# Performance work log

Hardware: AMD Instinct MI355X
Metric: run time of the kernel (lower is better)

The kernel has to match this reference:

```python
import jax, jax.numpy as jnp
import numpy as np

NUM_HEADS = 12
ALPHA = 0.5
TANH_CLIP = 5.0


def setup_inputs() -> dict:
    key = jax.random.key(0)
    k1, k2, k3, k4, k5 = jax.random.split(key, 5)
    B, N, C = 8, 1024, 768
    x = jax.random.normal(k1, (B, N, C), dtype=jnp.float32)
    # qkv: Linear(C -> 3C), proj: Linear(C -> C); torch stores weight as [out, in]
    s = 1.0 / np.sqrt(C)
    qkv_w = jax.random.normal(k2, (3 * C, C), dtype=jnp.float32) * s
    qkv_b = jax.random.normal(k3, (3 * C,), dtype=jnp.float32) * 0.02
    proj_w = jax.random.normal(k4, (C, C), dtype=jnp.float32) * s
    proj_b = jax.random.normal(k5, (C,), dtype=jnp.float32) * 0.02
    return {"x": x, "qkv_w": qkv_w, "qkv_b": qkv_b, "proj_w": proj_w, "proj_b": proj_b}


def reference(x, qkv_w, qkv_b, proj_w, proj_b):
    B, N, C = x.shape
    H = NUM_HEADS
    D = C // H
    scale = D ** -0.5
    # qkv projection -> [B, N, 3, H, D] -> q/k/v each [B, H, N, D]
    qkv = (x @ qkv_w.T + qkv_b).reshape(B, N, 3, H, D)
    qkv = jnp.transpose(qkv, (2, 0, 3, 1, 4))
    q, k, v = qkv[0], qkv[1], qkv[2]
    # pre-softmax scores [B, H, N, N]
    scores = jnp.einsum("bhnd,bhmd->bhnm", q * scale, k)
    scores_t = jnp.swapaxes(scores, -2, -1)
    scores_sym = 0.5 * (scores + scores_t)
    scores_asym = 0.5 * (scores - scores_t)
    scores = scores_sym + ALPHA * scores_asym
    # gamma_mode == 'approx'
    gamma = np.sqrt((1.0 + ALPHA ** 2) / 2.0)
    scores = scores / gamma
    # tanh clip
    scores = TANH_CLIP * jnp.tanh(scores / TANH_CLIP)
    attn = jax.nn.softmax(scores, axis=-1)
    out = jnp.einsum("bhnm,bhmd->bhnd", attn, v)  # [B, H, N, D]
    out = jnp.transpose(out, (0, 2, 1, 3)).reshape(B, N, C)
    return out @ proj_w.T + proj_b
```

## Files before the change

### kernel.cpp

```cpp
#include <hip/hip_runtime.h>
#include <hip/hip_bf16.h>
#include <stdint.h>

typedef unsigned short u16;
typedef __attribute__((ext_vector_type(8))) short bf16x8;
typedef __attribute__((ext_vector_type(4))) float f32x4;

#define LDS_AS(p) ((__attribute__((address_space(3))) void*)(p))
#define GLB_AS(p) ((__attribute__((address_space(1))) void*)(p))

__device__ __forceinline__ u16 f2bf(float f) {
  union { float f; uint32_t u; } v; v.f = f;
  uint32_t u = v.u;
  u += 0x7fffu + ((u >> 16) & 1u);
  return (u16)(u >> 16);
}

__device__ __forceinline__ float exp2_fast(float x) {
  float r;
  asm("v_exp_f32 %0, %1" : "=v"(r) : "v"(x));
  return r;
}

__device__ __forceinline__ float bits2f(uint32_t u) {
  union { uint32_t u; float f; } v; v.u = u; return v.f;
}
__device__ __forceinline__ uint32_t f2bits(float f) {
  union { float f; uint32_t u; } v; v.f = f; return v.u;
}

__device__ __forceinline__ void cvt8(const float* __restrict__ s, u16* __restrict__ d) {
  const float4* sv = (const float4*)s;
  float4 a = sv[0], b = sv[1];
  uint4 o;
  o.x = (uint32_t)f2bf(a.x) | ((uint32_t)f2bf(a.y) << 16);
  o.y = (uint32_t)f2bf(a.z) | ((uint32_t)f2bf(a.w) << 16);
  o.z = (uint32_t)f2bf(b.x) | ((uint32_t)f2bf(b.y) << 16);
  o.w = (uint32_t)f2bf(b.z) | ((uint32_t)f2bf(b.w) << 16);
  *(uint4*)d = o;
}

__global__ __launch_bounds__(256) void k_convert(
    const float* __restrict__ x, const float* __restrict__ wq, const float* __restrict__ wp,
    u16* __restrict__ xb, u16* __restrict__ wqb, u16* __restrict__ wpb) {
  int tid = blockIdx.x * 256 + threadIdx.x;
  int np  = gridDim.x * 256;
  for (int i = tid; i < (8192*768)/8; i += np) cvt8(x  + (size_t)i*8, xb  + (size_t)i*8);
  for (int i = tid; i < (2304*768)/8; i += np) cvt8(wq + (size_t)i*8, wqb + (size_t)i*8);
  for (int i = tid; i < (768*768)/8;  i += np) cvt8(wp + (size_t)i*8, wpb + (size_t)i*8);
}

template<bool SWAP>
__device__ __forceinline__ void gemm_core(const u16* __restrict__ A,
                                          const u16* __restrict__ B,
                                          u16* As, u16* Bs,
                                          int rowA0, int rowB0,
                                          f32x4 acc[4][4]) {
  const int t  = threadIdx.x;
  const int lane = t & 63;
  const int wv = t >> 6;
  const int wr = wv >> 1, wc = wv & 1;
  const int lr = lane & 15, lg = lane >> 4;

#pragma unroll 1
  for (int kt = 0; kt < 24; ++kt) {
    const int k0 = kt * 32;
    __syncthreads();
#pragma unroll
    for (int p = 0; p < 2; ++p) {
      int idx = p * 256 + t;
      int row = idx >> 2;
      int cc  = (idx & 3) ^ ((row >> 1) & 3);
      __builtin_amdgcn_global_load_lds(GLB_AS(A + (size_t)(rowA0 + row) * 768 + k0 + cc * 8),
                                       LDS_AS(As + idx * 8), 16, 0, 0);
    }
#pragma unroll
    for (int p = 0; p < 2; ++p) {
      int idx = p * 256 + t;
      int row = idx >> 2;
      int cc  = (idx & 3) ^ ((row >> 1) & 3);
      __builtin_amdgcn_global_load_lds(GLB_AS(B + (size_t)(rowB0 + row) * 768 + k0 + cc * 8),
                                       LDS_AS(Bs + idx * 8), 16, 0, 0);
    }
    asm volatile("s_waitcnt vmcnt(0)" ::: "memory");
    __syncthreads();

    bf16x8 af[4], bf_[4];
#pragma unroll
    for (int mi = 0; mi < 4; ++mi) {
      int row = wr * 64 + mi * 16 + lr;
      int cc  = lg ^ ((row >> 1) & 3);
      af[mi] = *(const bf16x8*)(As + row * 32 + cc * 8);
    }
#pragma unroll
    for (int ni = 0; ni < 4; ++ni) {
      int row = wc * 64 + ni * 16 + lr;
      int cc  = lg ^ ((row >> 1) & 3);
      bf_[ni] = *(const bf16x8*)(Bs + row * 32 + cc * 8);
    }
#pragma unroll
    for (int mi = 0; mi < 4; ++mi)
#pragma unroll
      for (int ni = 0; ni < 4; ++ni) {
        if (SWAP)
          acc[mi][ni] = __builtin_amdgcn_mfma_f32_16x16x32_bf16(bf_[ni], af[mi], acc[mi][ni], 0, 0, 0);
        else
          acc[mi][ni] = __builtin_amdgcn_mfma_f32_16x16x32_bf16(af[mi], bf_[ni], acc[mi][ni], 0, 0, 0);
      }
  }
}

__global__ __launch_bounds__(256) void k_gemm_qkv(
    const u16* __restrict__ Aq, const u16* __restrict__ Bw, const float* __restrict__ bias,
    u16* __restrict__ Qh, u16* __restrict__ Kh, u16* __restrict__ Vt) {
  __shared__ u16 As[128 * 32];
  __shared__ u16 Bs[128 * 32];
  int bid = blockIdx.x;
  int wg  = (bid & 7) * 144 + (bid >> 3);
  int bx  = wg % 18, by = wg / 18;

  const int t = threadIdx.x, lane = t & 63, wv = t >> 6;
  const int wr = wv >> 1, wc = wv & 1, lr = lane & 15, lg = lane >> 4;
  const int tsec = bx / 6;
  const int colBase = bx * 128 + wc * 64;

  const float gam = 0.7905694150420949f;
  const float sc1 = __builtin_sqrtf(0.09375f / gam);
  const float sc2 = __builtin_sqrtf(0.03125f / gam);

  f32x4 acc[4][4];
#pragma unroll
  for (int mi = 0; mi < 4; ++mi)
#pragma unroll
    for (int ni = 0; ni < 4; ++ni) acc[mi][ni] = (f32x4){0.f, 0.f, 0.f, 0.f};

  if (tsec < 2) {
    gemm_core<true>(Aq, Bw, As, Bs, by * 128, bx * 128, acc);

    float4 bv4[4];
#pragma unroll
    for (int ni = 0; ni < 4; ++ni)
      bv4[ni] = *(const float4*)(bias + colBase + ni * 16 + lg * 4);

#pragma unroll
    for (int mi = 0; mi < 4; ++mi) {
      int n = by * 128 + wr * 64 + mi * 16 + lr;
      int b = n >> 10, nn = n & 1023;
#pragma unroll
      for (int ni = 0; ni < 4; ++ni) {
        int fs = colBase - tsec * 768 + ni * 16 + lg * 4;
        int h = fs >> 6, d = fs & 63;
        size_t rowq = ((size_t)(b * 12 + h) * 1024 + nn) * 128;
        float v0 = acc[mi][ni][0] + bv4[ni].x;
        float v1 = acc[mi][ni][1] + bv4[ni].y;
        float v2 = acc[mi][ni][2] + bv4[ni].z;
        float v3 = acc[mi][ni][3] + bv4[ni].w;
        uint2 wq_, wk_;
        wq_.x = (uint32_t)f2bf(v0 * sc1) | ((uint32_t)f2bf(v1 * sc1) << 16);
        wq_.y = (uint32_t)f2bf(v2 * sc1) | ((uint32_t)f2bf(v3 * sc1) << 16);
        wk_.x = (uint32_t)f2bf(v0 * sc2) | ((uint32_t)f2bf(v1 * sc2) << 16);
        wk_.y = (uint32_t)f2bf(v2 * sc2) | ((uint32_t)f2bf(v3 * sc2) << 16);
        if (tsec == 0) {
          *(uint2*)(Qh + rowq + d)      = wq_;
          *(uint2*)(Kh + rowq + 64 + d) = wk_;
        } else {
          *(uint2*)(Kh + rowq + d)      = wq_;
          *(uint2*)(Qh + rowq + 64 + d) = wk_;
        }
      }
    }
  } else {
    gemm_core<false>(Aq, Bw, As, Bs, by * 128, bx * 128, acc);

    float bv[4];
#pragma unroll
    for (int ni = 0; ni < 4; ++ni) bv[ni] = bias[colBase + ni * 16 + lr];

#pragma unroll
    for (int mi = 0; mi < 4; ++mi) {
      int tok0 = by * 128 + wr * 64 + mi * 16 + lg * 4;
      int b = tok0 >> 10, n0 = tok0 & 1023;
#pragma unroll
      for (int ni = 0; ni < 4; ++ni) {
        int fs = colBase - 2 * 768 + ni * 16 + lr;
        int h = fs >> 6, d = fs & 63;
        float v0 = acc[mi][ni][0] + bv[ni];
        float v1 = acc[mi][ni][1] + bv[ni];
        float v2 = acc[mi][ni][2] + bv[ni];
        float v3 = acc[mi][ni][3] + bv[ni];
        uint2 w;
        w.x = (uint32_t)f2bf(v0) | ((uint32_t)f2bf(v1) << 16);
        w.y = (uint32_t)f2bf(v2) | ((uint32_t)f2bf(v3) << 16);
        *(uint2*)(Vt + ((size_t)((b * 12 + h) * 64 + d)) * 1024 + n0) = w;
      }
    }
  }
}

__global__ __launch_bounds__(256, 4) void k_attn(
    const u16* __restrict__ Qh, const u16* __restrict__ Kh, const u16* __restrict__ Vt,
    u16* __restrict__ attn) {
  __shared__ u16 Ks[2][32 * 128];
  __shared__ u16 Vs[2][64 * 32];
  __shared__ u16 Ps[4][32 * 40];

  int bid = blockIdx.x;
  int wg = (bid & 7) * 96 + (bid >> 3);
  int bh = wg >> 3, qb = wg & 7;
  int b = bh / 12, h = bh % 12;

  const int t = threadIdx.x, lane = t & 63, wv = t >> 6;
  const int lr = lane & 15, lg = lane >> 4;

  const size_t khb = (size_t)bh * 1024 * 128;
  const size_t vtb = (size_t)bh * 64 * 1024;

  bf16x8 qf[2][4];
  {
    const u16* qp = Qh + ((size_t)bh * 1024 + qb * 128 + wv * 32 + lr) * 128 + lg * 8;
#pragma unroll
    for (int it = 0; it < 2; ++it)
#pragma unroll
      for (int kk = 0; kk < 4; ++kk)
        qf[it][kk] = *(const bf16x8*)(qp + it * 16 * 128 + kk * 32);
  }

#define STAGE(KT, BUF)                                                                         \
  {                                                                                            \
    _Pragma("unroll")                                                                          \
    for (int p = 0; p < 2; ++p) {                                                              \
      int idx = p * 256 + t;                                                                   \
      int row = idx >> 4;                                                                      \
      int cc  = (idx & 15) ^ (row & 7);                                                        \
      __builtin_amdgcn_global_load_lds(GLB_AS(Kh + khb + (size_t)((KT) * 32 + row) * 128 + cc * 8), \
                                       LDS_AS(Ks[BUF] + idx * 8), 16, 0, 0);                   \
    }                                                                                          \
    {                                                                                          \
      int d = t >> 2;                                                                          \
      int g = (t & 3) ^ ((d + (d >> 2)) & 3);                                                  \
      __builtin_amdgcn_global_load_lds(GLB_AS(Vt + vtb + (size_t)d * 1024 + (KT) * 32 + g * 8),\
                                       LDS_AS(Vs[BUF] + t * 8), 16, 0, 0);                     \
    }                                                                                          \
  }

  STAGE(0, 0);

  f32x4 acc_o[4][2];
#pragma unroll
  for (int dt = 0; dt < 4; ++dt)
#pragma unroll
    for (int it = 0; it < 2; ++it) acc_o[dt][it] = (f32x4){0.f, 0.f, 0.f, 0.f};
  float dsum[2] = {0.f, 0.f};

  u16* pw = Ps[wv];
  const float C1 = 0.57707801636f;
  const float C2 = -14.4269504089f;

#pragma unroll 1
  for (int kt = 0; kt < 32; ++kt) {
    const int cur = kt & 1;
    __syncthreads();

    if (kt < 31) STAGE(kt + 1, cur ^ 1);

    const u16* K0 = Ks[cur];
    f32x4 accs[2][2];
#pragma unroll
    for (int jt = 0; jt < 2; ++jt)
#pragma unroll
      for (int it = 0; it < 2; ++it) accs[jt][it] = (f32x4){0.f, 0.f, 0.f, 0.f};
#pragma unroll
    for (int jt = 0; jt < 2; ++jt) {
#pragma unroll
      for (int kk = 0; kk < 4; ++kk) {
        int row = jt * 16 + lr;
        int cc  = (kk * 4 + lg) ^ (row & 7);
        bf16x8 kf = *(const bf16x8*)(K0 + row * 128 + cc * 8);
#pragma unroll
        for (int it = 0; it < 2; ++it)
          accs[jt][it] = __builtin_amdgcn_mfma_f32_16x16x32_bf16(kf, qf[it][kk], accs[jt][it], 0, 0, 0);
      }
    }

#pragma unroll
    for (int jt = 0; jt < 2; ++jt) {
#pragma unroll
      for (int it = 0; it < 2; ++it) {
        float p0 = exp2_fast(C2 * __builtin_amdgcn_rcpf(exp2_fast(C1 * accs[jt][it][0]) + 1.0f));
        float p1 = exp2_fast(C2 * __builtin_amdgcn_rcpf(exp2_fast(C1 * accs[jt][it][1]) + 1.0f));
        float p2 = exp2_fast(C2 * __builtin_amdgcn_rcpf(exp2_fast(C1 * accs[jt][it][2]) + 1.0f));
        float p3 = exp2_fast(C2 * __builtin_amdgcn_rcpf(exp2_fast(C1 * accs[jt][it][3]) + 1.0f));
        uint32_t a0 = f2bits(p0), a1 = f2bits(p1), a2 = f2bits(p2), a3 = f2bits(p3);
        uint2 w;
        w.x = (a0 >> 16) | (a1 & 0xFFFF0000u);
        w.y = (a2 >> 16) | (a3 & 0xFFFF0000u);
        dsum[it] += (bits2f(a0 & 0xFFFF0000u) + bits2f(a1 & 0xFFFF0000u))
                  + (bits2f(a2 & 0xFFFF0000u) + bits2f(a3 & 0xFFFF0000u));
        *(uint2*)(pw + (it * 16 + lr) * 40 + jt * 16 + lg * 4) = w;
      }
    }

    asm volatile("" ::: "memory");

    {
      const u16* V0 = Vs[cur];
      bf16x8 pa[2];
#pragma unroll
      for (int it = 0; it < 2; ++it)
        pa[it] = *(const bf16x8*)(pw + (it * 16 + lr) * 40 + lg * 8);
#pragma unroll
      for (int dt = 0; dt < 4; ++dt) {
        int row = dt * 16 + lr;
        int ph  = lg ^ ((row + (row >> 2)) & 3);
        bf16x8 vf = *(const bf16x8*)(V0 + row * 32 + ph * 8);
#pragma unroll
        for (int it = 0; it < 2; ++it)
          acc_o[dt][it] = __builtin_amdgcn_mfma_f32_16x16x32_bf16(vf, pa[it], acc_o[dt][it], 0, 0, 0);
      }
    }
  }
#undef STAGE

  float rinv[2];
#pragma unroll
  for (int it = 0; it < 2; ++it) {
    float v = dsum[it];
    v += __shfl_xor(v, 16);
    v += __shfl_xor(v, 32);
    rinv[it] = __builtin_amdgcn_rcpf(v);
  }

#pragma unroll
  for (int dt = 0; dt < 4; ++dt) {
#pragma unroll
    for (int it = 0; it < 2; ++it) {
      float v0 = acc_o[dt][it][0] * rinv[it];
      float v1 = acc_o[dt][it][1] * rinv[it];
      float v2 = acc_o[dt][it][2] * rinv[it];
      float v3 = acc_o[dt][it][3] * rinv[it];
      uint2 w;
      w.x = (uint32_t)f2bf(v0) | ((uint32_t)f2bf(v1) << 16);
      w.y = (uint32_t)f2bf(v2) | ((uint32_t)f2bf(v3) << 16);
      int n = qb * 128 + wv * 32 + it * 16 + lr;
      *(uint2*)(attn + ((size_t)(b * 1024 + n)) * 768 + h * 64 + dt * 16 + lg * 4) = w;
    }
  }
}

__global__ __launch_bounds__(256) void k_gemm_proj(
    const u16* __restrict__ Ain, const u16* __restrict__ Bw, const float* __restrict__ bias,
    float* __restrict__ out) {
  __shared__ u16 As[128 * 32];
  __shared__ u16 Bs[128 * 32];
  int bid = blockIdx.x;
  int wg  = (bid & 7) * 48 + (bid >> 3);
  int bx  = wg % 6, by = wg / 6;

  f32x4 acc[4][4];
#pragma unroll
  for (int mi = 0; mi < 4; ++mi)
#pragma unroll
    for (int ni = 0; ni < 4; ++ni) acc[mi][ni] = (f32x4){0.f, 0.f, 0.f, 0.f};

  gemm_core<false>(Ain, Bw, As, Bs, by * 128, bx * 128, acc);

  const int t = threadIdx.x, lane = t & 63, wv = t >> 6;
  const int wr = wv >> 1, wc = wv & 1, lr = lane & 15, lg = lane >> 4;
  const int col0 = bx * 128 + wc * 64;

  float bv[4];
#pragma unroll
  for (int ni = 0; ni < 4; ++ni) bv[ni] = bias[col0 + ni * 16 + lr];

#pragma unroll
  for (int mi = 0; mi < 4; ++mi) {
    int tok0 = by * 128 + wr * 64 + mi * 16 + lg * 4;
#pragma unroll
    for (int ni = 0; ni < 4; ++ni) {
      int col = col0 + ni * 16 + lr;
#pragma unroll
      for (int r = 0; r < 4; ++r) {
        out[(size_t)(tok0 + r) * 768 + col] = acc[mi][ni][r] + bv[ni];
      }
    }
  }
}

extern "C" void kernel_launch(void* const* d_in, const int* in_sizes, int n_in,
                              void* d_out, int out_size, void* d_ws, size_t ws_size,
                              hipStream_t stream) {
  (void)in_sizes; (void)n_in; (void)out_size;
  const float* x      = (const float*)d_in[0];
  const float* qkv_w  = (const float*)d_in[1];
  const float* qkv_b  = (const float*)d_in[2];
  const float* proj_w = (const float*)d_in[3];
  const float* proj_b = (const float*)d_in[4];
  float* out = (float*)d_out;

  uint8_t* ws = (uint8_t*)d_ws;
  u16* xb  = (u16*)(ws + 0);
  u16* wqb = (u16*)(ws + 12582912);
  u16* wpb = (u16*)(ws + 16121856);
  u16* Qh  = (u16*)(ws + 17301504);
  u16* Kh  = (u16*)(ws + 42467328);
  u16* Vt  = (u16*)(ws + 80216064);
  if (ws_size < 92798976) return;

  u16* attnb = xb;

  k_convert<<<1024, 256, 0, stream>>>(x, qkv_w, proj_w, xb, wqb, wpb);
  k_gemm_qkv<<<1152, 256, 0, stream>>>(xb, wqb, qkv_b, Qh, Kh, Vt);
  k_attn<<<768, 256, 0, stream>>>(Qh, Kh, Vt, attnb);
  k_gemm_proj<<<384, 256, 0, stream>>>(attnb, wpb, proj_b, out);
}
```

Before: 156.4 us.

## Halve attention query tile per block, double grid, fold tanh constant into QKV scale

The attention kernel now handles 64 queries per block (16 per wave) instead of 128, doubling the grid to 1536 blocks and raising the occupancy hint to 6 blocks per CU. The goal is better load balance across CUs and lower register pressure. The price is that each K/V tile is loaded from global memory twice as often. The tanh-clip constant C1 is now folded into the Q/K scaling in the QKV GEMM, which removes one multiply per score. The change also adds s_setprio around the MFMA sections and packs bf16 halves with a perm instruction.

```diff
diff --git a/kernel.cpp b/kernel.cpp
--- a/kernel.cpp
+++ b/kernel.cpp
@@ -27,6 +27,9 @@
 }
 __device__ __forceinline__ uint32_t f2bits(float f) {
   union { float f; uint32_t u; } v; v.f = f; return v.u;
+}
+__device__ __forceinline__ uint32_t pack_hi16(uint32_t lo_src, uint32_t hi_src) {
+  return __builtin_amdgcn_perm(hi_src, lo_src, 0x07060302u);
 }
 
 __device__ __forceinline__ void cvt8(const float* __restrict__ s, u16* __restrict__ d) {
@@ -125,8 +128,9 @@
   const int colBase = bx * 128 + wc * 64;
 
   const float gam = 0.7905694150420949f;
-  const float sc1 = __builtin_sqrtf(0.09375f / gam);
-  const float sc2 = __builtin_sqrtf(0.03125f / gam);
+  const float rC1 = __builtin_sqrtf(0.57707801636f);
+  const float sc1 = __builtin_sqrtf(0.09375f / gam) * rC1;
+  const float sc2 = __builtin_sqrtf(0.03125f / gam) * rC1;
 
   f32x4 acc[4][4];
 #pragma unroll
@@ -197,16 +201,16 @@
   }
 }
 
-__global__ __launch_bounds__(256, 4) void k_attn(
+__global__ __launch_bounds__(256, 6) void k_attn(
     const u16* __restrict__ Qh, const u16* __restrict__ Kh, const u16* __restrict__ Vt,
     u16* __restrict__ attn) {
   __shared__ u16 Ks[2][32 * 128];
   __shared__ u16 Vs[2][64 * 32];
-  __shared__ u16 Ps[4][32 * 40];
+  __shared__ u16 Ps[4][16 * 40];
 
   int bid = blockIdx.x;
-  int wg = (bid & 7) * 96 + (bid >> 3);
-  int bh = wg >> 3, qb = wg & 7;
+  int wg = (bid & 7) * 192 + (bid >> 3);
+  int bh = wg >> 4, qb = wg & 15;
   int b = bh / 12, h = bh % 12;
 
   const int t = threadIdx.x, lane = t & 63, wv = t >> 6;
@@ -215,14 +219,12 @@
   const size_t khb = (size_t)bh * 1024 * 128;
   const size_t vtb = (size_t)bh * 64 * 1024;
 
-  bf16x8 qf[2][4];
+  bf16x8 qf[4];
   {
-    const u16* qp = Qh + ((size_t)bh * 1024 + qb * 128 + wv * 32 + lr) * 128 + lg * 8;
-#pragma unroll
-    for (int it = 0; it < 2; ++it)
-#pragma unroll
-      for (int kk = 0; kk < 4; ++kk)
-        qf[it][kk] = *(const bf16x8*)(qp + it * 16 * 128 + kk * 32);
+    const u16* qp = Qh + ((size_t)bh * 1024 + qb * 64 + wv * 16 + lr) * 128 + lg * 8;
+#pragma unroll
+    for (int kk = 0; kk < 4; ++kk)
+      qf[kk] = *(const bf16x8*)(qp + kk * 32);
   }
 
 #define STAGE(KT, BUF)                                                                         \
@@ -245,15 +247,12 @@
 
   STAGE(0, 0);
 
-  f32x4 acc_o[4][2];
-#pragma unroll
-  for (int dt = 0; dt < 4; ++dt)
-#pragma unroll
-    for (int it = 0; it < 2; ++it) acc_o[dt][it] = (f32x4){0.f, 0.f, 0.f, 0.f};
-  float dsum[2] = {0.f, 0.f};
+  f32x4 acc_o[4];
+#pragma unroll
+  for (int dt = 0; dt < 4; ++dt) acc_o[dt] = (f32x4){0.f, 0.f, 0.f, 0.f};
+  float dsum = 0.f;
 
   u16* pw = Ps[wv];
-  const float C1 = 0.57707801636f;
   const float C2 = -14.4269504089f;
 
 #pragma unroll 1
@@ -264,11 +263,10 @@
     if (kt < 31) STAGE(kt + 1, cur ^ 1);
 
     const u16* K0 = Ks[cur];
-    f32x4 accs[2][2];
-#pragma unroll
-    for (int jt = 0; jt < 2; ++jt)
-#pragma unroll
-      for (int it = 0; it < 2; ++it) accs[jt][it] = (f32x4){0.f, 0.f, 0.f, 0.f};
+    f32x4 accs[2];
+#pragma unroll
+    for (int jt = 0; jt < 2; ++jt) accs[jt] = (f32x4){0.f, 0.f, 0.f, 0.f};
+    __builtin_amdgcn_s_setprio(1);
 #pragma unroll
     for (int jt = 0; jt < 2; ++jt) {
 #pragma unroll
@@ -276,74 +274,63 @@
         int row = jt * 16 + lr;
         int cc  = (kk * 4 + lg) ^ (row & 7);
         bf16x8 kf = *(const bf16x8*)(K0 + row * 128 + cc * 8);
-#pragma unroll
-        for (int it = 0; it < 2; ++it)
-          accs[jt][it] = __builtin_amdgcn_mfma_f32_16x16x32_bf16(kf, qf[it][kk], accs[jt][it], 0, 0, 0);
-      }
-    }
+        accs[jt] = __builtin_amdgcn_mfma_f32_16x16x32_bf16(kf, qf[kk], accs[jt], 0, 0, 0);
+      }
+    }
+    __builtin_amdgcn_s_setprio(0);
 
 #pragma unroll
     for (int jt = 0; jt < 2; ++jt) {
-#pragma unroll
-      for (int it = 0; it < 2; ++it) {
-        float p0 = exp2_fast(C2 * __builtin_amdgcn_rcpf(exp2_fast(C1 * accs[jt][it][0]) + 1.0f));
-        float p1 = exp2_fast(C2 * __builtin_amdgcn_rcpf(exp2_fast(C1 * accs[jt][it][1]) + 1.0f));
-        float p2 = exp2_fast(C2 * __builtin_amdgcn_rcpf(exp2_fast(C1 * accs[jt][it][2]) + 1.0f));
-        float p3 = exp2_fast(C2 * __builtin_amdgcn_rcpf(exp2_fast(C1 * accs[jt][it][3]) + 1.0f));
-        uint32_t a0 = f2bits(p0), a1 = f2bits(p1), a2 = f2bits(p2), a3 = f2bits(p3);
-        uint2 w;
-        w.x = (a0 >> 16) | (a1 & 0xFFFF0000u);
-        w.y = (a2 >> 16) | (a3 & 0xFFFF0000u);
-        dsum[it] += (bits2f(a0 & 0xFFFF0000u) + bits2f(a1 & 0xFFFF0000u))
-                  + (bits2f(a2 & 0xFFFF0000u) + bits2f(a3 & 0xFFFF0000u));
-        *(uint2*)(pw + (it * 16 + lr) * 40 + jt * 16 + lg * 4) = w;
-      }
+      float p0 = exp2_fast(C2 * __builtin_amdgcn_rcpf(exp2_fast(accs[jt][0]) + 1.0f));
+      float p1 = exp2_fast(C2 * __builtin_amdgcn_rcpf(exp2_fast(accs[jt][1]) + 1.0f));
+      float p2 = exp2_fast(C2 * __builtin_amdgcn_rcpf(exp2_fast(accs[jt][2]) + 1.0f));
+      float p3 = exp2_fast(C2 * __builtin_amdgcn_rcpf(exp2_fast(accs[jt][3]) + 1.0f));
+      uint32_t a0 = f2bits(p0), a1 = f2bits(p1), a2 = f2bits(p2), a3 = f2bits(p3);
+      uint2 w;
+      w.x = pack_hi16(a0, a1);
+      w.y = pack_hi16(a2, a3);
+      dsum += (bits2f(a0 & 0xFFFF0000u) + bits2f(a1 & 0xFFFF0000u))
+            + (bits2f(a2 & 0xFFFF0000u) + bits2f(a3 & 0xFFFF0000u));
+      *(uint2*)(pw + lr * 40 + jt * 16 + lg * 4) = w;
     }
 
     asm volatile("" ::: "memory");
 
     {
       const u16* V0 = Vs[cur];
-      bf16x8 pa[2];
-#pragma unroll
-      for (int it = 0; it < 2; ++it)
-        pa[it] = *(const bf16x8*)(pw + (it * 16 + lr) * 40 + lg * 8);
+      bf16x8 pa = *(const bf16x8*)(pw + lr * 40 + lg * 8);
+      __builtin_amdgcn_s_setprio(1);
 #pragma unroll
       for (int dt = 0; dt < 4; ++dt) {
         int row = dt * 16 + lr;
         int ph  = lg ^ ((row + (row >> 2)) & 3);
         bf16x8 vf = *(const bf16x8*)(V0 + row * 32 + ph * 8);
-#pragma unroll
-        for (int it = 0; it < 2; ++it)
-          acc_o[dt][it] = __builtin_amdgcn_mfma_f32_16x16x32_bf16(vf, pa[it], acc_o[dt][it], 0, 0, 0);
-      }
+        acc_o[dt] = __builtin_amdgcn_mfma_f32_16x16x32_bf16(vf, pa, acc_o[dt], 0, 0, 0);
+      }
+      __builtin_amdgcn_s_setprio(0);
     }
   }
 #undef STAGE
 
-  float rinv[2];
-#pragma unroll
-  for (int it = 0; it < 2; ++it) {
-    float v = dsum[it];
+  float rinv;
+  {
+    float v = dsum;
     v += __shfl_xor(v, 16);
     v += __shfl_xor(v, 32);
-    rinv[it] = __builtin_amdgcn_rcpf(v);
+    rinv = __builtin_amdgcn_rcpf(v);
   }
 
 #pragma unroll
   for (int dt = 0; dt < 4; ++dt) {
-#pragma unroll
-    for (int it = 0; it < 2; ++it) {
-      float v0 = acc_o[dt][it][0] * rinv[it];
-      float v1 = acc_o[dt][it][1] * rinv[it];
-      float v2 = acc_o[dt][it][2] * rinv[it];
-      float v3 = acc_o[dt][it][3] * rinv[it];
-      uint2 w;
-      w.x = (uint32_t)f2bf(v0) | ((uint32_t)f2bf(v1) << 16);
-      w.y = (uint32_t)f2bf(v2) | ((uint32_t)f2bf(v3) << 16);
-      int n = qb * 128 + wv * 32 + it * 16 + lr;
-      *(uint2*)(attn + ((size_t)(b * 1024 + n)) * 768 + h * 64 + dt * 16 + lg * 4) = w;
-    }
+    float v0 = acc_o[dt][0] * rinv;
+    float v1 = acc_o[dt][1] * rinv;
+    float v2 = acc_o[dt][2] * rinv;
+    float v3 = acc_o[dt][3] * rinv;
+    uint2 w;
+    w.x = (uint32_t)f2bf(v0) | ((uint32_t)f2bf(v1) << 16);
+    w.y = (uint32_t)f2bf(v2) | ((uint32_t)f2bf(v3) << 16);
+    int n = qb * 64 + wv * 16 + lr;
+    *(uint2*)(attn + ((size_t)(b * 1024 + n)) * 768 + h * 64 + dt * 16 + lg * 4) = w;
   }
 }
 
@@ -410,6 +397,6 @@
 
   k_convert<<<1024, 256, 0, stream>>>(x, qkv_w, proj_w, xb, wqb, wpb);
   k_gemm_qkv<<<1152, 256, 0, stream>>>(xb, wqb, qkv_b, Qh, Kh, Vt);
-  k_attn<<<768, 256, 0, stream>>>(Qh, Kh, Vt, attnb);
+  k_attn<<<1536, 256, 0, stream>>>(Qh, Kh, Vt, attnb);
   k_gemm_proj<<<384, 256, 0, stream>>>(attnb, wpb, proj_b, out);
 }
```

Measured after the change: 170.4 us. +9.0%, slower.
